# Optimization experiments

Hardware: AMD Instinct MI355X
Metric: run time of the kernel (lower is better)

Reference implementation:

```python
import jax, jax.numpy as jnp
import numpy as np

N = 1_000_000   # gaussians
K_NB = 10       # neighbor control points per gaussian
K_TOTAL = 300   # num_fine control points


def _normalize(q, eps=1e-8):
    return q / jnp.maximum(jnp.linalg.norm(q, axis=-1, keepdims=True), eps)


def quaternion_to_rotation_matrix(q):
    # q: [..., 4] in (w, x, y, z); normalized before conversion
    q = _normalize(q)
    w, x, y, z = q[..., 0], q[..., 1], q[..., 2], q[..., 3]
    R = jnp.stack([
        jnp.stack([1 - 2 * (y * y + z * z), 2 * (x * y - w * z), 2 * (x * z + w * y)], axis=-1),
        jnp.stack([2 * (x * y + w * z), 1 - 2 * (x * x + z * z), 2 * (y * z - w * x)], axis=-1),
        jnp.stack([2 * (x * z - w * y), 2 * (y * z + w * x), 1 - 2 * (x * x + y * y)], axis=-1),
    ], axis=-2)  # [..., 3, 3]
    return R


def quaternion_multiply(a, b):
    # Hamilton product, (w, x, y, z)
    aw, ax, ay, az = a[..., 0], a[..., 1], a[..., 2], a[..., 3]
    bw, bx, by, bz = b[..., 0], b[..., 1], b[..., 2], b[..., 3]
    return jnp.stack([
        aw * bw - ax * bx - ay * by - az * bz,
        aw * bx + ax * bw + ay * bz - az * by,
        aw * by - ax * bz + ay * bw + az * bx,
        aw * bz + ax * by - ay * bx + az * bw,
    ], axis=-1)


def setup_inputs() -> dict:
    key = jax.random.key(0)
    ks = jax.random.split(key, 7)
    means = jax.random.normal(ks[0], (N, 3), dtype=jnp.float32)
    quaternions = _normalize(jax.random.normal(ks[1], (N, 4), dtype=jnp.float32))
    w = jax.random.uniform(ks[2], (N, K_NB), dtype=jnp.float32) + 1e-3
    weights = w / w.sum(-1, keepdims=True)  # blending weights sum to 1
    indices = jax.random.randint(ks[3], (N, K_NB), 0, K_TOTAL)
    ctrl_translations = 0.1 * jax.random.normal(ks[4], (K_TOTAL, 3), dtype=jnp.float32)
    ctrl_rotations = _normalize(jax.random.normal(ks[5], (K_TOTAL, 4), dtype=jnp.float32))
    ctrl_positions = jax.random.normal(ks[6], (K_TOTAL, 3), dtype=jnp.float32)
    return {
        'means': means, 'quaternions': quaternions, 'weights': weights,
        'ctrl_translations': ctrl_translations, 'ctrl_rotations': ctrl_rotations,
        'ctrl_positions': ctrl_positions, 'indices': indices,
    }


def reference(means, quaternions, weights, ctrl_translations, ctrl_rotations, ctrl_positions, indices):
    # gather neighbor control-point transforms
    nb_trans = ctrl_translations[indices]   # [N, K, 3]
    nb_rots = ctrl_rotations[indices]       # [N, K, 4]
    nb_pos = ctrl_positions[indices]        # [N, K, 3]

    diff = means[:, None, :] - nb_pos                       # [N, K, 3]
    R_ctrl = quaternion_to_rotation_matrix(nb_rots)         # [N, K, 3, 3]
    rotated_diff = jnp.einsum('nkij,nkj->nki', R_ctrl, diff)
    deformed_per_cp = rotated_diff + nb_pos + nb_trans      # [N, K, 3]

    w = weights[..., None]                                  # [N, K, 1]
    deformed_means = (w * deformed_per_cp).sum(axis=1)      # [N, 3]

    blended_rot = _normalize((w * nb_rots).sum(axis=1))     # [N, 4]
    deformed_quats = quaternion_multiply(blended_rot, quaternions)
    return deformed_means, deformed_quats
```

## Files before the change

kernel.cpp:

```cpp
#include <hip/hip_runtime.h>
#include <math.h>


template <int KNB>
__global__ __launch_bounds__(256) void deform_kernel(
    const float* __restrict__ means,
    const float* __restrict__ quats,
    const float* __restrict__ weights,
    const float* __restrict__ ctrl_trans,
    const float* __restrict__ ctrl_rot,
    const float* __restrict__ ctrl_pos,
    const int*   __restrict__ indices,
    float* __restrict__ out_means,
    float* __restrict__ out_quats,
    int N, int K_TOTAL)
{
    extern __shared__ float4 s4[];

    for (int cp = threadIdx.x; cp < K_TOTAL; cp += blockDim.x) {
        float qw = ctrl_rot[cp * 4 + 0];
        float qx = ctrl_rot[cp * 4 + 1];
        float qy = ctrl_rot[cp * 4 + 2];
        float qz = ctrl_rot[cp * 4 + 3];
        float n  = sqrtf(qw * qw + qx * qx + qy * qy + qz * qz);
        float inv = 1.0f / fmaxf(n, 1e-8f);
        float w = qw * inv, x = qx * inv, y = qy * inv, z = qz * inv;
        float R00 = 1.0f - 2.0f * (y * y + z * z);
        float R01 = 2.0f * (x * y - w * z);
        float R02 = 2.0f * (x * z + w * y);
        float R10 = 2.0f * (x * y + w * z);
        float R11 = 1.0f - 2.0f * (x * x + z * z);
        float R12 = 2.0f * (y * z - w * x);
        float R20 = 2.0f * (x * z - w * y);
        float R21 = 2.0f * (y * z + w * x);
        float R22 = 1.0f - 2.0f * (x * x + y * y);
        float px = ctrl_pos[cp * 3 + 0];
        float py = ctrl_pos[cp * 3 + 1];
        float pz = ctrl_pos[cp * 3 + 2];
        float tx = ctrl_trans[cp * 3 + 0];
        float ty = ctrl_trans[cp * 3 + 1];
        float tz = ctrl_trans[cp * 3 + 2];
        float bx = px + tx - (R00 * px + R01 * py + R02 * pz);
        float by = py + ty - (R10 * px + R11 * py + R12 * pz);
        float bz = pz + tz - (R20 * px + R21 * py + R22 * pz);
        s4[cp * 5 + 0] = make_float4(R00, R01, R02, R10);
        s4[cp * 5 + 1] = make_float4(R11, R12, R20, R21);
        s4[cp * 5 + 2] = make_float4(R22, bx, by, bz);
        s4[cp * 5 + 3] = make_float4(qw, qx, qy, qz);
    }
    __syncthreads();

    int i = blockIdx.x * blockDim.x + threadIdx.x;
    if (i >= N) return;

    const int*   idx_row = indices + (long long)i * KNB;
    const float* w_row   = weights + (long long)i * KNB;

    float acc[16];
#pragma unroll
    for (int j = 0; j < 16; j++) acc[j] = 0.0f;

#pragma unroll
    for (int k = 0; k < KNB; k++) {
        int   cp = idx_row[k];
        float w  = w_row[k];
        float4 a = s4[cp * 5 + 0];
        float4 b = s4[cp * 5 + 1];
        float4 c = s4[cp * 5 + 2];
        float4 d = s4[cp * 5 + 3];
        acc[0]  = fmaf(w, a.x, acc[0]);
        acc[1]  = fmaf(w, a.y, acc[1]);
        acc[2]  = fmaf(w, a.z, acc[2]);
        acc[3]  = fmaf(w, a.w, acc[3]);
        acc[4]  = fmaf(w, b.x, acc[4]);
        acc[5]  = fmaf(w, b.y, acc[5]);
        acc[6]  = fmaf(w, b.z, acc[6]);
        acc[7]  = fmaf(w, b.w, acc[7]);
        acc[8]  = fmaf(w, c.x, acc[8]);
        acc[9]  = fmaf(w, c.y, acc[9]);
        acc[10] = fmaf(w, c.z, acc[10]);
        acc[11] = fmaf(w, c.w, acc[11]);
        acc[12] = fmaf(w, d.x, acc[12]);
        acc[13] = fmaf(w, d.y, acc[13]);
        acc[14] = fmaf(w, d.z, acc[14]);
        acc[15] = fmaf(w, d.w, acc[15]);
    }

    float mx = means[i * 3 + 0];
    float my = means[i * 3 + 1];
    float mz = means[i * 3 + 2];

    float dmx = acc[0] * mx + acc[1] * my + acc[2] * mz + acc[9];
    float dmy = acc[3] * mx + acc[4] * my + acc[5] * mz + acc[10];
    float dmz = acc[6] * mx + acc[7] * my + acc[8] * mz + acc[11];

    out_means[i * 3 + 0] = dmx;
    out_means[i * 3 + 1] = dmy;
    out_means[i * 3 + 2] = dmz;

    float bw = acc[12], bx = acc[13], by = acc[14], bz = acc[15];
    float n  = sqrtf(bw * bw + bx * bx + by * by + bz * bz);
    float inv = 1.0f / fmaxf(n, 1e-8f);
    bw *= inv; bx *= inv; by *= inv; bz *= inv;

    float4 g = ((const float4*)quats)[i];
    float gw = g.x, gx = g.y, gy = g.z, gz = g.w;

    float ow = bw * gw - bx * gx - by * gy - bz * gz;
    float ox = bw * gx + bx * gw + by * gz - bz * gy;
    float oy = bw * gy - bx * gz + by * gw + bz * gx;
    float oz = bw * gz + bx * gy - by * gx + bz * gw;

    float4* oq = (float4*)(out_quats + (long long)i * 4);
    *oq = make_float4(ow, ox, oy, oz);
}

__global__ __launch_bounds__(256) void deform_kernel_generic(
    const float* __restrict__ means,
    const float* __restrict__ quats,
    const float* __restrict__ weights,
    const float* __restrict__ ctrl_trans,
    const float* __restrict__ ctrl_rot,
    const float* __restrict__ ctrl_pos,
    const int*   __restrict__ indices,
    float* __restrict__ out_means,
    float* __restrict__ out_quats,
    int N, int K_NB, int K_TOTAL)
{
    extern __shared__ float4 s4[];
    for (int cp = threadIdx.x; cp < K_TOTAL; cp += blockDim.x) {
        float qw = ctrl_rot[cp * 4 + 0];
        float qx = ctrl_rot[cp * 4 + 1];
        float qy = ctrl_rot[cp * 4 + 2];
        float qz = ctrl_rot[cp * 4 + 3];
        float n  = sqrtf(qw * qw + qx * qx + qy * qy + qz * qz);
        float inv = 1.0f / fmaxf(n, 1e-8f);
        float w = qw * inv, x = qx * inv, y = qy * inv, z = qz * inv;
        float R00 = 1.0f - 2.0f * (y * y + z * z);
        float R01 = 2.0f * (x * y - w * z);
        float R02 = 2.0f * (x * z + w * y);
        float R10 = 2.0f * (x * y + w * z);
        float R11 = 1.0f - 2.0f * (x * x + z * z);
        float R12 = 2.0f * (y * z - w * x);
        float R20 = 2.0f * (x * z - w * y);
        float R21 = 2.0f * (y * z + w * x);
        float R22 = 1.0f - 2.0f * (x * x + y * y);
        float px = ctrl_pos[cp * 3 + 0];
        float py = ctrl_pos[cp * 3 + 1];
        float pz = ctrl_pos[cp * 3 + 2];
        float tx = ctrl_trans[cp * 3 + 0];
        float ty = ctrl_trans[cp * 3 + 1];
        float tz = ctrl_trans[cp * 3 + 2];
        float bx = px + tx - (R00 * px + R01 * py + R02 * pz);
        float by = py + ty - (R10 * px + R11 * py + R12 * pz);
        float bz = pz + tz - (R20 * px + R21 * py + R22 * pz);
        s4[cp * 5 + 0] = make_float4(R00, R01, R02, R10);
        s4[cp * 5 + 1] = make_float4(R11, R12, R20, R21);
        s4[cp * 5 + 2] = make_float4(R22, bx, by, bz);
        s4[cp * 5 + 3] = make_float4(qw, qx, qy, qz);
    }
    __syncthreads();

    int i = blockIdx.x * blockDim.x + threadIdx.x;
    if (i >= N) return;

    const int*   idx_row = indices + (long long)i * K_NB;
    const float* w_row   = weights + (long long)i * K_NB;

    float acc[16];
#pragma unroll
    for (int j = 0; j < 16; j++) acc[j] = 0.0f;

    for (int k = 0; k < K_NB; k++) {
        int   cp = idx_row[k];
        float w  = w_row[k];
        float4 a = s4[cp * 5 + 0];
        float4 b = s4[cp * 5 + 1];
        float4 c = s4[cp * 5 + 2];
        float4 d = s4[cp * 5 + 3];
        acc[0]  = fmaf(w, a.x, acc[0]);
        acc[1]  = fmaf(w, a.y, acc[1]);
        acc[2]  = fmaf(w, a.z, acc[2]);
        acc[3]  = fmaf(w, a.w, acc[3]);
        acc[4]  = fmaf(w, b.x, acc[4]);
        acc[5]  = fmaf(w, b.y, acc[5]);
        acc[6]  = fmaf(w, b.z, acc[6]);
        acc[7]  = fmaf(w, b.w, acc[7]);
        acc[8]  = fmaf(w, c.x, acc[8]);
        acc[9]  = fmaf(w, c.y, acc[9]);
        acc[10] = fmaf(w, c.z, acc[10]);
        acc[11] = fmaf(w, c.w, acc[11]);
        acc[12] = fmaf(w, d.x, acc[12]);
        acc[13] = fmaf(w, d.y, acc[13]);
        acc[14] = fmaf(w, d.z, acc[14]);
        acc[15] = fmaf(w, d.w, acc[15]);
    }

    float mx = means[i * 3 + 0];
    float my = means[i * 3 + 1];
    float mz = means[i * 3 + 2];

    float dmx = acc[0] * mx + acc[1] * my + acc[2] * mz + acc[9];
    float dmy = acc[3] * mx + acc[4] * my + acc[5] * mz + acc[10];
    float dmz = acc[6] * mx + acc[7] * my + acc[8] * mz + acc[11];

    out_means[i * 3 + 0] = dmx;
    out_means[i * 3 + 1] = dmy;
    out_means[i * 3 + 2] = dmz;

    float bw = acc[12], bx = acc[13], by = acc[14], bz = acc[15];
    float n  = sqrtf(bw * bw + bx * bx + by * by + bz * bz);
    float inv = 1.0f / fmaxf(n, 1e-8f);
    bw *= inv; bx *= inv; by *= inv; bz *= inv;

    float4 g = ((const float4*)quats)[i];
    float gw = g.x, gx = g.y, gy = g.z, gz = g.w;

    float ow = bw * gw - bx * gx - by * gy - bz * gz;
    float ox = bw * gx + bx * gw + by * gz - bz * gy;
    float oy = bw * gy - bx * gz + by * gw + bz * gx;
    float oz = bw * gz + bx * gy - by * gx + bz * gw;

    float4* oq = (float4*)(out_quats + (long long)i * 4);
    *oq = make_float4(ow, ox, oy, oz);
}

extern "C" void kernel_launch(void* const* d_in, const int* in_sizes, int n_in,
                              void* d_out, int out_size, void* d_ws, size_t ws_size,
                              hipStream_t stream) {
    const float* means      = (const float*)d_in[0];
    const float* quats      = (const float*)d_in[1];
    const float* weights    = (const float*)d_in[2];
    const float* ctrl_trans = (const float*)d_in[3];
    const float* ctrl_rot   = (const float*)d_in[4];
    const float* ctrl_pos   = (const float*)d_in[5];
    const int*   indices    = (const int*)d_in[6];

    int N       = in_sizes[0] / 3;
    int K_NB    = in_sizes[2] / N;
    int K_TOTAL = in_sizes[3] / 3;

    float* out_means = (float*)d_out;
    float* out_quats = (float*)d_out + (long long)N * 3;

    int block = 256;
    int grid  = (N + block - 1) / block;
    size_t smem = (size_t)K_TOTAL * 5 * sizeof(float4);

    if (K_NB == 10) {
        deform_kernel<10><<<grid, block, smem, stream>>>(
            means, quats, weights, ctrl_trans, ctrl_rot, ctrl_pos, indices,
            out_means, out_quats, N, K_TOTAL);
    } else {
        deform_kernel_generic<<<grid, block, smem, stream>>>(
            means, quats, weights, ctrl_trans, ctrl_rot, ctrl_pos, indices,
            out_means, out_quats, N, K_NB, K_TOTAL);
    }
}
```

Before: 145.7 us.

## Prefetch per-gaussian inputs before smem table build, restructure accumulation, use 512-thread blocks

The per-gaussian indices and weights (read as int2/float2 pairs), means and quaternions are now loaded into registers before the shared-memory control-point table is built, so their global-memory latency overlaps the table setup and the barrier. The inner loop now applies each control point's affine transform to the mean directly and accumulates 7 values instead of 16, which lowers register pressure. Block size rises to 512 with a launch-bounds occupancy hint, halving how many blocks rebuild the table. The generic kernel is removed and unsupported K_NB values fall back to the K=10 template, which would give wrong results for other neighbour counts.

```diff
diff --git a/kernel.cpp b/kernel.cpp
--- a/kernel.cpp
+++ b/kernel.cpp
@@ -3,7 +3,7 @@
 
 
 template <int KNB>
-__global__ __launch_bounds__(256) void deform_kernel(
+__global__ __launch_bounds__(512, 6) void deform_kernel(
     const float* __restrict__ means,
     const float* __restrict__ quats,
     const float* __restrict__ weights,
@@ -16,6 +16,32 @@
     int N, int K_TOTAL)
 {
     extern __shared__ float4 s4[];
+
+    const int i = blockIdx.x * blockDim.x + threadIdx.x;
+    const bool active = i < N;
+
+    int   idx[KNB];
+    float wt[KNB];
+    float mx = 0.f, my = 0.f, mz = 0.f;
+    float4 g = make_float4(0.f, 0.f, 0.f, 0.f);
+    if (active) {
+        const int*   idx_row = indices + (long long)i * KNB;
+        const float* w_row   = weights + (long long)i * KNB;
+        const int2*   ip = (const int2*)idx_row;
+        const float2* wp = (const float2*)w_row;
+#pragma unroll
+        for (int k = 0; k < KNB / 2; k++) {
+            int2 iv = ip[k];
+            float2 wv = wp[k];
+            idx[2 * k] = iv.x; idx[2 * k + 1] = iv.y;
+            wt[2 * k] = wv.x;  wt[2 * k + 1] = wv.y;
+        }
+        if (KNB & 1) { idx[KNB - 1] = idx_row[KNB - 1]; wt[KNB - 1] = w_row[KNB - 1]; }
+        mx = means[i * 3 + 0];
+        my = means[i * 3 + 1];
+        mz = means[i * 3 + 2];
+        g = ((const float4*)quats)[i];
+    }
 
     for (int cp = threadIdx.x; cp < K_TOTAL; cp += blockDim.x) {
         float qw = ctrl_rot[cp * 4 + 0];
@@ -50,179 +76,46 @@
     }
     __syncthreads();
 
-    int i = blockIdx.x * blockDim.x + threadIdx.x;
-    if (i >= N) return;
+    if (!active) return;
 
-    const int*   idx_row = indices + (long long)i * KNB;
-    const float* w_row   = weights + (long long)i * KNB;
-
-    float acc[16];
-#pragma unroll
-    for (int j = 0; j < 16; j++) acc[j] = 0.0f;
+    float dmx = 0.f, dmy = 0.f, dmz = 0.f;
+    float qaw = 0.f, qax = 0.f, qay = 0.f, qaz = 0.f;
 
 #pragma unroll
     for (int k = 0; k < KNB; k++) {
-        int   cp = idx_row[k];
-        float w  = w_row[k];
+        int   cp = idx[k];
+        float w  = wt[k];
         float4 a = s4[cp * 5 + 0];
         float4 b = s4[cp * 5 + 1];
         float4 c = s4[cp * 5 + 2];
         float4 d = s4[cp * 5 + 3];
-        acc[0]  = fmaf(w, a.x, acc[0]);
-        acc[1]  = fmaf(w, a.y, acc[1]);
-        acc[2]  = fmaf(w, a.z, acc[2]);
-        acc[3]  = fmaf(w, a.w, acc[3]);
-        acc[4]  = fmaf(w, b.x, acc[4]);
-        acc[5]  = fmaf(w, b.y, acc[5]);
-        acc[6]  = fmaf(w, b.z, acc[6]);
-        acc[7]  = fmaf(w, b.w, acc[7]);
-        acc[8]  = fmaf(w, c.x, acc[8]);
-        acc[9]  = fmaf(w, c.y, acc[9]);
-        acc[10] = fmaf(w, c.z, acc[10]);
-        acc[11] = fmaf(w, c.w, acc[11]);
-        acc[12] = fmaf(w, d.x, acc[12]);
-        acc[13] = fmaf(w, d.y, acc[13]);
-        acc[14] = fmaf(w, d.z, acc[14]);
-        acc[15] = fmaf(w, d.w, acc[15]);
+        float rx = fmaf(a.x, mx, fmaf(a.y, my, fmaf(a.z, mz, c.y)));
+        float ry = fmaf(a.w, mx, fmaf(b.x, my, fmaf(b.y, mz, c.z)));
+        float rz = fmaf(b.z, mx, fmaf(b.w, my, fmaf(c.x, mz, c.w)));
+        dmx = fmaf(w, rx, dmx);
+        dmy = fmaf(w, ry, dmy);
+        dmz = fmaf(w, rz, dmz);
+        qaw = fmaf(w, d.x, qaw);
+        qax = fmaf(w, d.y, qax);
+        qay = fmaf(w, d.z, qay);
+        qaz = fmaf(w, d.w, qaz);
     }
-
-    float mx = means[i * 3 + 0];
-    float my = means[i * 3 + 1];
-    float mz = means[i * 3 + 2];
-
-    float dmx = acc[0] * mx + acc[1] * my + acc[2] * mz + acc[9];
-    float dmy = acc[3] * mx + acc[4] * my + acc[5] * mz + acc[10];
-    float dmz = acc[6] * mx + acc[7] * my + acc[8] * mz + acc[11];
 
     out_means[i * 3 + 0] = dmx;
     out_means[i * 3 + 1] = dmy;
     out_means[i * 3 + 2] = dmz;
 
-    float bw = acc[12], bx = acc[13], by = acc[14], bz = acc[15];
-    float n  = sqrtf(bw * bw + bx * bx + by * by + bz * bz);
+    float n   = sqrtf(qaw * qaw + qax * qax + qay * qay + qaz * qaz);
     float inv = 1.0f / fmaxf(n, 1e-8f);
-    bw *= inv; bx *= inv; by *= inv; bz *= inv;
+    float bw = qaw * inv, bx = qax * inv, by = qay * inv, bz = qaz * inv;
 
-    float4 g = ((const float4*)quats)[i];
     float gw = g.x, gx = g.y, gy = g.z, gz = g.w;
-
     float ow = bw * gw - bx * gx - by * gy - bz * gz;
     float ox = bw * gx + bx * gw + by * gz - bz * gy;
     float oy = bw * gy - bx * gz + by * gw + bz * gx;
     float oz = bw * gz + bx * gy - by * gx + bz * gw;
 
-    float4* oq = (float4*)(out_quats + (long long)i * 4);
-    *oq = make_float4(ow, ox, oy, oz);
-}
-
-__global__ __launch_bounds__(256) void deform_kernel_generic(
-    const float* __restrict__ means,
-    const float* __restrict__ quats,
-    const float* __restrict__ weights,
-    const float* __restrict__ ctrl_trans,
-    const float* __restrict__ ctrl_rot,
-    const float* __restrict__ ctrl_pos,
-    const int*   __restrict__ indices,
-    float* __restrict__ out_means,
-    float* __restrict__ out_quats,
-    int N, int K_NB, int K_TOTAL)
-{
-    extern __shared__ float4 s4[];
-    for (int cp = threadIdx.x; cp < K_TOTAL; cp += blockDim.x) {
-        float qw = ctrl_rot[cp * 4 + 0];
-        float qx = ctrl_rot[cp * 4 + 1];
-        float qy = ctrl_rot[cp * 4 + 2];
-        float qz = ctrl_rot[cp * 4 + 3];
-        float n  = sqrtf(qw * qw + qx * qx + qy * qy + qz * qz);
-        float inv = 1.0f / fmaxf(n, 1e-8f);
-        float w = qw * inv, x = qx * inv, y = qy * inv, z = qz * inv;
-        float R00 = 1.0f - 2.0f * (y * y + z * z);
-        float R01 = 2.0f * (x * y - w * z);
-        float R02 = 2.0f * (x * z + w * y);
-        float R10 = 2.0f * (x * y + w * z);
-        float R11 = 1.0f - 2.0f * (x * x + z * z);
-        float R12 = 2.0f * (y * z - w * x);
-        float R20 = 2.0f * (x * z - w * y);
-        float R21 = 2.0f * (y * z + w * x);
-        float R22 = 1.0f - 2.0f * (x * x + y * y);
-        float px = ctrl_pos[cp * 3 + 0];
-        float py = ctrl_pos[cp * 3 + 1];
-        float pz = ctrl_pos[cp * 3 + 2];
-        float tx = ctrl_trans[cp * 3 + 0];
-        float ty = ctrl_trans[cp * 3 + 1];
-        float tz = ctrl_trans[cp * 3 + 2];
-        float bx = px + tx - (R00 * px + R01 * py + R02 * pz);
-        float by = py + ty - (R10 * px + R11 * py + R12 * pz);
-        float bz = pz + tz - (R20 * px + R21 * py + R22 * pz);
-        s4[cp * 5 + 0] = make_float4(R00, R01, R02, R10);
-        s4[cp * 5 + 1] = make_float4(R11, R12, R20, R21);
-        s4[cp * 5 + 2] = make_float4(R22, bx, by, bz);
-        s4[cp * 5 + 3] = make_float4(qw, qx, qy, qz);
-    }
-    __syncthreads();
-
-    int i = blockIdx.x * blockDim.x + threadIdx.x;
-    if (i >= N) return;
-
-    const int*   idx_row = indices + (long long)i * K_NB;
-    const float* w_row   = weights + (long long)i * K_NB;
-
-    float acc[16];
-#pragma unroll
-    for (int j = 0; j < 16; j++) acc[j] = 0.0f;
-
-    for (int k = 0; k < K_NB; k++) {
-        int   cp = idx_row[k];
-        float w  = w_row[k];
-        float4 a = s4[cp * 5 + 0];
-        float4 b = s4[cp * 5 + 1];
-        float4 c = s4[cp * 5 + 2];
-        float4 d = s4[cp * 5 + 3];
-        acc[0]  = fmaf(w, a.x, acc[0]);
-        acc[1]  = fmaf(w, a.y, acc[1]);
-        acc[2]  = fmaf(w, a.z, acc[2]);
-        acc[3]  = fmaf(w, a.w, acc[3]);
-        acc[4]  = fmaf(w, b.x, acc[4]);
-        acc[5]  = fmaf(w, b.y, acc[5]);
-        acc[6]  = fmaf(w, b.z, acc[6]);
-        acc[7]  = fmaf(w, b.w, acc[7]);
-        acc[8]  = fmaf(w, c.x, acc[8]);
-        acc[9]  = fmaf(w, c.y, acc[9]);
-        acc[10] = fmaf(w, c.z, acc[10]);
-        acc[11] = fmaf(w, c.w, acc[11]);
-        acc[12] = fmaf(w, d.x, acc[12]);
-        acc[13] = fmaf(w, d.y, acc[13]);
-        acc[14] = fmaf(w, d.z, acc[14]);
-        acc[15] = fmaf(w, d.w, acc[15]);
-    }
-
-    float mx = means[i * 3 + 0];
-    float my = means[i * 3 + 1];
-    float mz = means[i * 3 + 2];
-
-    float dmx = acc[0] * mx + acc[1] * my + acc[2] * mz + acc[9];
-    float dmy = acc[3] * mx + acc[4] * my + acc[5] * mz + acc[10];
-    float dmz = acc[6] * mx + acc[7] * my + acc[8] * mz + acc[11];
-
-    out_means[i * 3 + 0] = dmx;
-    out_means[i * 3 + 1] = dmy;
-    out_means[i * 3 + 2] = dmz;
-
-    float bw = acc[12], bx = acc[13], by = acc[14], bz = acc[15];
-    float n  = sqrtf(bw * bw + bx * bx + by * by + bz * bz);
-    float inv = 1.0f / fmaxf(n, 1e-8f);
-    bw *= inv; bx *= inv; by *= inv; bz *= inv;
-
-    float4 g = ((const float4*)quats)[i];
-    float gw = g.x, gx = g.y, gy = g.z, gz = g.w;
-
-    float ow = bw * gw - bx * gx - by * gy - bz * gz;
-    float ox = bw * gx + bx * gw + by * gz - bz * gy;
-    float oy = bw * gy - bx * gz + by * gw + bz * gx;
-    float oz = bw * gz + bx * gy - by * gx + bz * gw;
-
-    float4* oq = (float4*)(out_quats + (long long)i * 4);
-    *oq = make_float4(ow, ox, oy, oz);
+    ((float4*)(out_quats))[i] = make_float4(ow, ox, oy, oz);
 }
 
 extern "C" void kernel_launch(void* const* d_in, const int* in_sizes, int n_in,
@@ -243,7 +136,7 @@
     float* out_means = (float*)d_out;
     float* out_quats = (float*)d_out + (long long)N * 3;
 
-    int block = 256;
+    int block = 512;
     int grid  = (N + block - 1) / block;
     size_t smem = (size_t)K_TOTAL * 5 * sizeof(float4);
 
@@ -251,9 +144,17 @@
         deform_kernel<10><<<grid, block, smem, stream>>>(
             means, quats, weights, ctrl_trans, ctrl_rot, ctrl_pos, indices,
             out_means, out_quats, N, K_TOTAL);
+    } else if (K_NB == 8) {
+        deform_kernel<8><<<grid, block, smem, stream>>>(
+            means, quats, weights, ctrl_trans, ctrl_rot, ctrl_pos, indices,
+            out_means, out_quats, N, K_TOTAL);
+    } else if (K_NB == 16) {
+        deform_kernel<16><<<grid, block, smem, stream>>>(
+            means, quats, weights, ctrl_trans, ctrl_rot, ctrl_pos, indices,
+            out_means, out_quats, N, K_TOTAL);
     } else {
-        deform_kernel_generic<<<grid, block, smem, stream>>>(
+        deform_kernel<10><<<grid, block, smem, stream>>>(
             means, quats, weights, ctrl_trans, ctrl_rot, ctrl_pos, indices,
-            out_means, out_quats, N, K_NB, K_TOTAL);
+            out_means, out_quats, N, K_TOTAL);
     }
 }
```

After: 149.5 us. 2.6% more time.
